# Kernel tuning notes

Measured on AMD Instinct MI355X. Metric: run time of the kernel, lower is better.

The kernel has to match this reference:

```python
import jax, jax.numpy as jnp
import numpy as np

T = 16          # time_span
N = 128         # num_trajectory
D = 512         # embedding dim
TEMP = 0.1      # temperature
INF = 1000000000.0
M = 2 * N * T   # total rows of z (two views)


def setup_inputs() -> dict:
    key = jax.random.key(0)
    k1, k2 = jax.random.split(key)
    z = jax.random.normal(k1, (M, D), dtype=jnp.float32)
    done = jax.random.randint(k2, (T, N), 0, 2).astype(jnp.int32)  # [T, N] binary done flags
    return {"z": z, "done": done}


def _build_positive_mask(done):
    # done: [T, N] int -> transposed to [N, T] as in the torch code
    d = done.astype(jnp.float32).T  # [N, T]
    # Sequential rewrite loop is equivalent to:
    #   done_new[r,t] = 1 iff exists original done at p < t in row r AND orig done[r,t] == 0
    excl = jnp.cumsum(d, axis=1) - d  # exclusive cumsum along time
    d_new = jnp.where((excl > 0) & (d == 0), 1.0, 0.0)  # [N, T]
    done_vec = 1.0 - d_new.reshape(-1)  # [N*T]
    # block-diagonal temporal mask: same trajectory => 1
    traj = jnp.arange(N * T) // T
    block = (traj[:, None] == traj[None, :]).astype(jnp.float32)  # [NT, NT]
    done_mask = (done_vec[:, None] * done_vec[None, :]) * block
    done_mask = jnp.tile(done_mask, (2, 2))      # [M, M]
    temporal_mask = jnp.tile(block, (2, 2))      # [M, M]
    eye = jnp.eye(M, dtype=jnp.float32)
    positive_mask = (1.0 - done_mask) * (1.0 - temporal_mask) + eye
    return positive_mask, eye


def reference(z, done):
    positive_mask, eye = _build_positive_mask(done)
    # cosine similarity = normalize + GEMM (same math as broadcasted F.cosine_similarity)
    norms = jnp.maximum(jnp.linalg.norm(z, axis=-1, keepdims=True), 1e-8)
    zn = z / norms
    logits = (zn @ zn.T) / TEMP - eye * INF  # [M, M]
    log_probs = jax.nn.log_softmax(logits, axis=1)
    neg = 1.0 - positive_mask
    mean_log_prob = jnp.sum(neg * log_probs, axis=1) / jnp.sum(neg, axis=1)
    return -jnp.mean(mean_log_prob)
```

## Files before the change

### kernel.cpp

```cpp
#include <hip/hip_runtime.h>
#include <hip/hip_bf16.h>

typedef __bf16 bf16x8 __attribute__((ext_vector_type(8)));
typedef float f32x16 __attribute__((ext_vector_type(16)));
typedef unsigned int u32x4 __attribute__((ext_vector_type(4)));
typedef unsigned short u16;


__global__ void nrm_kernel(const float* __restrict__ z, u16* __restrict__ zn) {
    int tid = threadIdx.x;
    int l = tid & 63, w = tid >> 6;
    int row = blockIdx.x * 4 + w;
    const float4* src = (const float4*)(z + row * 512);
    float4 v0 = src[l];
    float4 v1 = src[l + 64];
    float ss = v0.x * v0.x + v0.y * v0.y + v0.z * v0.z + v0.w * v0.w
             + v1.x * v1.x + v1.y * v1.y + v1.z * v1.z + v1.w * v1.w;
#pragma unroll
    for (int off = 32; off; off >>= 1) ss += __shfl_xor(ss, off, 64);
    float sc = 1.0f / fmaxf(sqrtf(ss), 1e-8f);
    __hip_bfloat16 b0[4], b1[4];
    b0[0] = __float2bfloat16(v0.x * sc); b0[1] = __float2bfloat16(v0.y * sc);
    b0[2] = __float2bfloat16(v0.z * sc); b0[3] = __float2bfloat16(v0.w * sc);
    b1[0] = __float2bfloat16(v1.x * sc); b1[1] = __float2bfloat16(v1.y * sc);
    b1[2] = __float2bfloat16(v1.z * sc); b1[3] = __float2bfloat16(v1.w * sc);
    uint2 p0, p1;
    __builtin_memcpy(&p0, b0, 8);
    __builtin_memcpy(&p1, b1, 8);
    ((uint2*)(zn + row * 512))[l] = p0;
    ((uint2*)(zn + row * 512))[l + 64] = p1;
}

__global__ __launch_bounds__(256, 1) void gemm_kernel(const u16* __restrict__ zn,
                                                      float* __restrict__ merged,
                                                      float* __restrict__ possum) {
    __shared__ u16 Bt[2][32 * 512];

    int tid = threadIdx.x;
    int wave = tid >> 6;
    int l = tid & 63;
    int m = l & 31, h = l >> 5;

    if (blockIdx.x >= 528) {
        if (tid < 64) {
            int g = blockIdx.x - 528;
            int grow = (m < 16) ? (g * 16 + m) : (2048 + g * 16 + (m - 16));
            const u32x4* src = (const u32x4*)(zn + grow * 512);
            f32x16 acc = {};
#pragma unroll
            for (int kc = 0; kc < 32; ++kc) {
                bf16x8 f = __builtin_bit_cast(bf16x8, src[h + 2 * kc]);
                acc = __builtin_amdgcn_mfma_f32_32x32x16_bf16(f, f, acc, 0, 0, 0);
            }
#pragma unroll
            for (int r = 0; r < 16; ++r) {
                int rrow = (r & 3) + 8 * (r >> 2) + 4 * h;
                float v = (rrow == m) ? 0.f : acc[r];
                v += __shfl_xor(v, 1, 64);
                v += __shfl_xor(v, 2, 64);
                v += __shfl_xor(v, 4, 64);
                v += __shfl_xor(v, 8, 64);
                v += __shfl_xor(v, 16, 64);
                if (m == 0) {
                    int gr = (rrow < 16) ? (g * 16 + rrow) : (2048 + g * 16 + (rrow - 16));
                    possum[gr] = v * 10.0f;
                }
            }
        }
        return;
    }

    int b = blockIdx.x;
    int ti = 0;
    while (b >= 32 - ti) { b -= 32 - ti; ++ti; }
    int tj = ti + b;

    int rowbase = ti * 128 + wave * 32;
    int colbase = tj * 128;
    bool diag = (ti == tj);

    u32x4 a[32];
    const u32x4* arow = (const u32x4*)(zn + (rowbase + m) * 512);
#pragma unroll
    for (int kc = 0; kc < 32; ++kc) a[kc] = arow[h + 2 * kc];

    float racc[16];
#pragma unroll
    for (int r = 0; r < 16; ++r) racc[r] = 0.f;
    float colacc[4] = {0.f, 0.f, 0.f, 0.f};

    int c = tid >> 3, g0 = tid & 7;
    int wbase = (g0 >> 1) * 1024 + (g0 & 1) * 512 + c * 16;
    const u32x4* zsrc = (const u32x4*)(zn + (colbase + c) * 512);

    u32x4 stg[8];
    {
#pragma unroll
        for (int i = 0; i < 8; ++i) stg[i] = zsrc[g0 + 8 * i];
        char* dst = (char*)Bt[0] + wbase;
#pragma unroll
        for (int i = 0; i < 8; ++i) *(u32x4*)(dst + i * 4096) = stg[i];
    }
    __syncthreads();

#pragma unroll
    for (int ct = 0; ct < 4; ++ct) {
        if (ct < 3) {
            const u32x4* nsrc = zsrc + (ct + 1) * 2048;
#pragma unroll
            for (int i = 0; i < 8; ++i) stg[i] = nsrc[g0 + 8 * i];
        }
        const char* rb = (const char*)Bt[ct & 1] + l * 16;
        f32x16 acc = {};
#pragma unroll
        for (int kc = 0; kc < 32; ++kc) {
            bf16x8 bf = *(const bf16x8*)(rb + kc * 1024);
            acc = __builtin_amdgcn_mfma_f32_32x32x16_bf16(
                __builtin_bit_cast(bf16x8, a[kc]), bf, acc, 0, 0, 0);
        }

        if (diag && ct == wave) {
#pragma unroll
            for (int r = 0; r < 16; ++r) {
                int rrow = (r & 3) + 8 * (r >> 2) + 4 * h;
                if (rrow != m) racc[r] += __builtin_exp2f(acc[r] * 14.426950408889634f);
            }
        } else {
            float csum = 0.f;
#pragma unroll
            for (int r = 0; r < 16; ++r) {
                float e = __builtin_exp2f(acc[r] * 14.426950408889634f);
                racc[r] += e;
                csum += e;
            }
            colacc[ct] += csum;
        }

        if (ct < 3) {
            char* dst = (char*)Bt[(ct + 1) & 1] + wbase;
#pragma unroll
            for (int i = 0; i < 8; ++i) *(u32x4*)(dst + i * 4096) = stg[i];
        }
        __syncthreads();
    }

#pragma unroll
    for (int r = 0; r < 16; ++r) {
        float v = racc[r];
        v += __shfl_xor(v, 1, 64);
        v += __shfl_xor(v, 2, 64);
        v += __shfl_xor(v, 4, 64);
        v += __shfl_xor(v, 8, 64);
        v += __shfl_xor(v, 16, 64);
        if (m == 0) {
            int rrow = (r & 3) + 8 * (r >> 2) + 4 * h;
            merged[(rowbase + rrow) * 32 + tj] = v;
        }
    }

    if (!diag) {
        float* colred = (float*)Bt;
#pragma unroll
        for (int ct = 0; ct < 4; ++ct) {
            float v = colacc[ct] + __shfl_xor(colacc[ct], 32, 64);
            if (h == 0) colred[wave * 128 + ct * 32 + m] = v;
        }
        __syncthreads();
        if (tid < 128) {
            float s = colred[tid] + colred[128 + tid] + colred[256 + tid] + colred[384 + tid];
            merged[(colbase + tid) * 32 + ti] = s;
        }
    }
}

__global__ void finA_kernel(const float* __restrict__ merged,
                            const float* __restrict__ possum,
                            float* __restrict__ partial) {
    int tid = threadIdx.x;
    int r = blockIdx.x * 256 + tid;
    const float4* mrow = (const float4*)(merged + r * 32);
    float s = 0.f;
#pragma unroll
    for (int i = 0; i < 8; ++i) {
        float4 v = mrow[i];
        s += (v.x + v.y) + (v.z + v.w);
    }
    float loss = __logf(s) - possum[r] * (1.0f / 31.0f);
#pragma unroll
    for (int off = 32; off; off >>= 1) loss += __shfl_xor(loss, off, 64);
    __shared__ float red[4];
    if ((tid & 63) == 0) red[tid >> 6] = loss;
    __syncthreads();
    if (tid == 0) partial[blockIdx.x] = (red[0] + red[1]) + (red[2] + red[3]);
}

__global__ void finB_kernel(const float* __restrict__ partial, float* __restrict__ out) {
    int l = threadIdx.x;
    float v = (l < 16) ? partial[l] : 0.f;
    v += __shfl_xor(v, 1, 64);
    v += __shfl_xor(v, 2, 64);
    v += __shfl_xor(v, 4, 64);
    v += __shfl_xor(v, 8, 64);
    if (l == 0) out[0] = v * (1.0f / 4096.0f);
}

extern "C" void kernel_launch(void* const* d_in, const int* in_sizes, int n_in,
                              void* d_out, int out_size, void* d_ws, size_t ws_size,
                              hipStream_t stream) {
    const float* z = (const float*)d_in[0];
    u16* zn = (u16*)d_ws;
    float* merged = (float*)((char*)d_ws + (4u << 20));
    float* possum = merged + 4096 * 32;
    float* partial = possum + 4096;
    float* out = (float*)d_out;

    nrm_kernel<<<1024, 256, 0, stream>>>(z, zn);
    gemm_kernel<<<656, 256, 0, stream>>>(zn, merged, possum);
    finA_kernel<<<16, 256, 0, stream>>>(merged, possum, partial);
    finB_kernel<<<1, 64, 0, stream>>>(partial, out);
}
```

Before: 108.8 us.

## Raise GEMM occupancy by dropping register-resident A and LDS double buffer

The GEMM kernel no longer keeps the whole 32x512 A row slice in 128 VGPRs and no longer double-buffers B in LDS. A is re-read from global/L2 in chunks of eight inside each column-tile pass, B uses a single 32KB LDS buffer with extra barriers, and launch bounds ask for 4 blocks per CU. The goal is more resident waves to hide latency, at the cost of reloading A four times and losing the prefetch overlap of B loads with MFMA work.

Result: slower. 120.9 us (+11.1%).

```diff
diff --git a/kernel.cpp b/kernel.cpp
--- a/kernel.cpp
+++ b/kernel.cpp
@@ -31,10 +31,10 @@
     ((uint2*)(zn + row * 512))[l + 64] = p1;
 }
 
-__global__ __launch_bounds__(256, 1) void gemm_kernel(const u16* __restrict__ zn,
+__global__ __launch_bounds__(256, 4) void gemm_kernel(const u16* __restrict__ zn,
                                                       float* __restrict__ merged,
                                                       float* __restrict__ possum) {
-    __shared__ u16 Bt[2][32 * 512];
+    __shared__ u16 Bt[32 * 512];
 
     int tid = threadIdx.x;
     int wave = tid >> 6;
@@ -79,10 +79,7 @@
     int colbase = tj * 128;
     bool diag = (ti == tj);
 
-    u32x4 a[32];
     const u32x4* arow = (const u32x4*)(zn + (rowbase + m) * 512);
-#pragma unroll
-    for (int kc = 0; kc < 32; ++kc) a[kc] = arow[h + 2 * kc];
 
     float racc[16];
 #pragma unroll
@@ -92,31 +89,32 @@
     int c = tid >> 3, g0 = tid & 7;
     int wbase = (g0 >> 1) * 1024 + (g0 & 1) * 512 + c * 16;
     const u32x4* zsrc = (const u32x4*)(zn + (colbase + c) * 512);
-
-    u32x4 stg[8];
-    {
-#pragma unroll
-        for (int i = 0; i < 8; ++i) stg[i] = zsrc[g0 + 8 * i];
-        char* dst = (char*)Bt[0] + wbase;
-#pragma unroll
-        for (int i = 0; i < 8; ++i) *(u32x4*)(dst + i * 4096) = stg[i];
-    }
-    __syncthreads();
+    const char* rb = (const char*)Bt + l * 16;
 
 #pragma unroll
     for (int ct = 0; ct < 4; ++ct) {
-        if (ct < 3) {
-            const u32x4* nsrc = zsrc + (ct + 1) * 2048;
-#pragma unroll
-            for (int i = 0; i < 8; ++i) stg[i] = nsrc[g0 + 8 * i];
-        }
-        const char* rb = (const char*)Bt[ct & 1] + l * 16;
+        if (ct) __syncthreads();
+        {
+            const u32x4* src = zsrc + ct * 2048;
+            char* dst = (char*)Bt + wbase;
+#pragma unroll
+            for (int i = 0; i < 8; ++i) *(u32x4*)(dst + i * 4096) = src[g0 + 8 * i];
+        }
+        __syncthreads();
+
         f32x16 acc = {};
 #pragma unroll
-        for (int kc = 0; kc < 32; ++kc) {
-            bf16x8 bf = *(const bf16x8*)(rb + kc * 1024);
-            acc = __builtin_amdgcn_mfma_f32_32x32x16_bf16(
-                __builtin_bit_cast(bf16x8, a[kc]), bf, acc, 0, 0, 0);
+        for (int o = 0; o < 4; ++o) {
+            u32x4 ap[8];
+#pragma unroll
+            for (int j = 0; j < 8; ++j) ap[j] = arow[h + 16 * o + 2 * j];
+#pragma unroll
+            for (int j = 0; j < 8; ++j) {
+                int kc = 8 * o + j;
+                bf16x8 bf = *(const bf16x8*)(rb + kc * 1024);
+                acc = __builtin_amdgcn_mfma_f32_32x32x16_bf16(
+                    __builtin_bit_cast(bf16x8, ap[j]), bf, acc, 0, 0, 0);
+            }
         }
 
         if (diag && ct == wave) {
@@ -135,13 +133,6 @@
             }
             colacc[ct] += csum;
         }
-
-        if (ct < 3) {
-            char* dst = (char*)Bt[(ct + 1) & 1] + wbase;
-#pragma unroll
-            for (int i = 0; i < 8; ++i) *(u32x4*)(dst + i * 4096) = stg[i];
-        }
-        __syncthreads();
     }
 
 #pragma unroll
@@ -159,6 +150,7 @@
     }
 
     if (!diag) {
+        __syncthreads();
         float* colred = (float*)Bt;
 #pragma unroll
         for (int ct = 0; ct < 4; ++ct) {
```
